# Optimization experiments

Hardware: AMD Instinct MI355X
Metric: run time of the kernel (lower is better)

## Reference

```python
import jax, jax.numpy as jnp
import numpy as np


def setup_inputs() -> dict:
    key = jax.random.key(0)
    kp, ka = jax.random.split(key)
    N, A = 100000, 1024
    # points: xyz over a 100m x 100m plot, z in [0, 30] (tree heights)
    u = jax.random.uniform(kp, (N, 3), dtype=jnp.float32)
    points = u * jnp.array([100.0, 100.0, 30.0], dtype=jnp.float32)
    # anchors: [cx, cy, cz, w, l, h]
    ua = jax.random.uniform(ka, (A, 6), dtype=jnp.float32)
    cx = ua[:, 0] * 100.0
    cy = ua[:, 1] * 100.0
    cz = jnp.zeros((A,), jnp.float32)
    w = 2.0 + ua[:, 3] * 6.0
    l = 2.0 + ua[:, 4] * 6.0
    h = 10.0 + ua[:, 5] * 20.0
    anchors = jnp.stack([cx, cy, cz, w, l, h], axis=1)
    return {"points": points, "anchors": anchors, "n": 512}


def _roi_point_pool(points, anchors, n):
    """Vectorised per-anchor point-in-box pooling (TreeRCNN._subsample_points_batch).

    Returns padded [A, n, 3] anchor-local points (x,y translated by anchor
    center, z untouched) and per-anchor clamped counts. Slots >= count are 0.
    Selection of the first-n in-box points is deterministic in point order
    (the torch code uses a random tie-break key; determinism chosen for a
    reproducible correctness baseline — same gather/scatter structure).
    """
    A = anchors.shape[0]
    N = points.shape[0]
    px, py, pz = points[:, 0], points[:, 1], points[:, 2]
    cx, cy = anchors[:, 0:1], anchors[:, 1:2]
    w, l, h = anchors[:, 3:4], anchors[:, 4:5], anchors[:, 5:6]
    # [A, N] box-membership mask (the O(A*N) traffic-bound hot loop)
    mask = ((px >= cx - w * 0.5) & (px <= cx + w * 0.5)
            & (py >= cy - l * 0.5) & (py <= cy + l * 0.5)
            & (pz >= 0.0) & (pz <= h))
    # per-anchor local slot index for each in-box point
    local = jnp.cumsum(mask.astype(jnp.int32), axis=1) - 1          # [A, N]
    valid = mask & (local < n)
    counts = valid.sum(axis=1)                                      # [A]
    # scatter point ids (+1 so 0 marks empty) into flat padded slots;
    # invalid hits go to a dump slot A*n
    flat = jnp.where(valid,
                     jnp.arange(A, dtype=jnp.int32)[:, None] * n + local,
                     A * n)
    vals = (jnp.arange(N, dtype=jnp.int32)[None, :] + 1) * valid
    pid = jnp.zeros(A * n + 1, jnp.int32).at[flat.reshape(-1)].add(vals.reshape(-1))
    pid = pid[: A * n].reshape(A, n)                                # [A, n]
    points_ext = jnp.concatenate([jnp.zeros((1, 3), points.dtype), points], axis=0)
    padded = points_ext[pid]                                        # [A, n, 3]
    # translate x,y to anchor-local coords on filled slots only
    centers = jnp.concatenate([anchors[:, :2], jnp.zeros((A, 1), anchors.dtype)], axis=1)
    padded = jnp.where(pid[..., None] > 0, padded - centers[:, None, :], 0.0)
    return padded, counts


def reference(points, anchors, n):
    return _roi_point_pool(points, anchors, n)
```

## Files before the change

### kernel.cpp

```cpp
#include <hip/hip_runtime.h>


#define NB     128
#define NBB    (NB * NB)
#define CAPB   32
#define NWRD   3584
#define WPT    7
#define MAXBIN 160

__global__ __launch_bounds__(256) void scatter_kernel(
    const float* __restrict__ pts, unsigned int* __restrict__ bincnt,
    float4* __restrict__ bucket, const unsigned int* __restrict__ pbase, int N)
{
    const int i = blockIdx.x * 256 + threadIdx.x;
    if (i >= N) return;
    const unsigned int P = *pbase;
    const float px = pts[3 * i + 0], py = pts[3 * i + 1], pz = pts[3 * i + 2];
    const float s = NB / 100.0f;
    const int bx = min(NB - 1, (int)(px * s));
    const int by = min(NB - 1, (int)(py * s));
    const int bin = by * NB + bx;
    const unsigned int slot = atomicAdd(&bincnt[bin], 1u) - P;
    if (slot < CAPB)
        bucket[bin * CAPB + slot] = make_float4(px, py, pz, __int_as_float(i));
}

__global__ __launch_bounds__(512) void anchor_kernel(
    const float* __restrict__ pts, const float* __restrict__ anc,
    const unsigned int* __restrict__ bincnt, const float4* __restrict__ bucket,
    const unsigned int* __restrict__ pbase,
    float* __restrict__ out_pts, float* __restrict__ out_cnt, int n)
{
    const int a    = blockIdx.x;
    const int tid  = threadIdx.x;
    const int lane = tid & 63;
    const int wave = tid >> 6;

    const float cx = anc[a * 6 + 0], cy = anc[a * 6 + 1];
    const float w  = anc[a * 6 + 3], l  = anc[a * 6 + 4], h = anc[a * 6 + 5];
    const float xl = cx - w * 0.5f, xh = cx + w * 0.5f;
    const float yl = cy - l * 0.5f, yh = cy + l * 0.5f;

    __shared__ unsigned int s_mask[NWRD];
    __shared__ int s_bcnt[MAXBIN];
    __shared__ int s_wsum[8], s_wpre[9];

    #pragma unroll
    for (int u = 0; u < WPT; ++u) s_mask[tid + u * 512] = 0u;

    const unsigned int P = *pbase;
    const float sc = NB / 100.0f;
    const int bx0 = max(0, (int)floorf(xl * sc));
    const int bx1 = min(NB - 1, (int)floorf(xh * sc));
    const int by0 = max(0, (int)floorf(yl * sc));
    const int by1 = min(NB - 1, (int)floorf(yh * sc));
    const int nbx = bx1 - bx0 + 1;
    const int nby = by1 - by0 + 1;
    const int nbins = (nbx > 0 && nby > 0) ? nbx * nby : 0;

    for (int t = tid; t < nbins; t += 512) {
        const int by = by0 + t / nbx, bx = bx0 + t % nbx;
        s_bcnt[t] = min((int)(bincnt[by * NB + bx] - P), CAPB);
    }
    __syncthreads();

    const int totB = nbins * 8;
    for (int t = tid; t < totB; t += 512) {
        const int slot = t & 7;
        const int b    = t >> 3;
        const int cnt  = s_bcnt[b];
        const int bin  = (by0 + b / nbx) * NB + bx0 + b % nbx;
        const float4 p = bucket[bin * CAPB + slot];
        if (slot < cnt &&
            p.x >= xl && p.x <= xh && p.y >= yl && p.y <= yh &&
            p.z >= 0.0f && p.z <= h) {
            const int idx = __float_as_int(p.w);
            atomicOr(&s_mask[idx >> 5], 1u << (idx & 31));
        }
    }

    const int totC = nbins * 24;
    for (int t = tid; t < totC; t += 512) {
        const int b    = t / 24;
        const int slot = 8 + t - b * 24;
        const int cnt  = s_bcnt[b];
        if (slot < cnt) {
            const int bin  = (by0 + b / nbx) * NB + bx0 + b % nbx;
            const float4 p = bucket[bin * CAPB + slot];
            if (p.x >= xl && p.x <= xh && p.y >= yl && p.y <= yh &&
                p.z >= 0.0f && p.z <= h) {
                const int idx = __float_as_int(p.w);
                atomicOr(&s_mask[idx >> 5], 1u << (idx & 31));
            }
        }
    }
    __syncthreads();

    const int wbase = tid * WPT;
    int s = 0;
    unsigned int mw[WPT];
    #pragma unroll
    for (int u = 0; u < WPT; ++u) {
        mw[u] = s_mask[wbase + u];
        s += __popc(mw[u]);
    }
    int incl = s;
    #pragma unroll
    for (int d = 1; d < 64; d <<= 1) {
        const int t = __shfl_up(incl, d);
        if (lane >= d) incl += t;
    }
    if (lane == 63) s_wsum[wave] = incl;
    __syncthreads();
    if (tid == 0) {
        int run = 0;
        #pragma unroll
        for (int v = 0; v < 8; ++v) { const int t = s_wsum[v]; s_wpre[v] = run; run += t; }
        s_wpre[8] = run;
    }
    __syncthreads();
    const int total = s_wpre[8];
    const int count = total < n ? total : n;
    int slot = s_wpre[wave] + incl - s;

    float* const outa = out_pts + (size_t)a * n * 3;
    #pragma unroll
    for (int u = 0; u < WPT; ++u) {
        unsigned int wm = mw[u];
        while (wm) {
            const int b = __ffs(wm) - 1;
            wm &= wm - 1u;
            if (slot < n) {
                const int i = (wbase + u) * 32 + b;
                outa[3 * slot + 0] = pts[3 * i + 0] - cx;
                outa[3 * slot + 1] = pts[3 * i + 1] - cy;
                outa[3 * slot + 2] = pts[3 * i + 2];
            }
            ++slot;
        }
    }

    for (int t = count * 3 + tid; t < n * 3; t += 512) outa[t] = 0.f;
    if (tid == 0) out_cnt[a] = (float)count;
}

__global__ __launch_bounds__(256) void roi_pool_kernel(
    const float* __restrict__ pts, const float* __restrict__ anc,
    float* __restrict__ out_pts, float* __restrict__ out_cnt, int N, int n)
{
    const int a = blockIdx.x;
    const float cx = anc[a * 6 + 0], cy = anc[a * 6 + 1];
    const float w  = anc[a * 6 + 3], l  = anc[a * 6 + 4], h = anc[a * 6 + 5];
    const float xmin = cx - 0.5f * w, xmax = cx + 0.5f * w;
    const float ymin = cy - 0.5f * l, ymax = cy + 0.5f * l;
    const int tid = threadIdx.x, wave = tid >> 6, lane = tid & 63;
    __shared__ int s_tot[4];
    int base = 0;
    float* const outa = out_pts + (size_t)a * n * 3;
    for (int start = 0; start < N; start += 256) {
        const int i = start + tid;
        bool m = false;
        float px = 0.f, py = 0.f, pz = 0.f;
        if (i < N) {
            px = pts[3 * i]; py = pts[3 * i + 1]; pz = pts[3 * i + 2];
            m = (px >= xmin) & (px <= xmax) & (py >= ymin) & (py <= ymax) &
                (pz >= 0.0f) & (pz <= h);
        }
        const unsigned long long ball = __ballot(m);
        const int lanePfx = __popcll(ball & ((1ull << lane) - 1ull));
        if (lane == 0) s_tot[wave] = __popcll(ball);
        __syncthreads();
        const int t0 = s_tot[0], t1 = s_tot[1], t2 = s_tot[2], t3 = s_tot[3];
        int offs = base;
        if (wave > 0) offs += t0;
        if (wave > 1) offs += t1;
        if (wave > 2) offs += t2;
        const int slot = offs + lanePfx;
        if (m && slot < n) {
            float* o = outa + (size_t)slot * 3;
            o[0] = px - cx; o[1] = py - cy; o[2] = pz;
        }
        base += t0 + t1 + t2 + t3;
        __syncthreads();
        if (base >= n) break;
    }
    const int count = base < n ? base : n;
    if (tid == 0) out_cnt[a] = (float)count;
    for (int s = count + tid; s < n; s += 256) {
        float* o = outa + (size_t)s * 3;
        o[0] = 0.f; o[1] = 0.f; o[2] = 0.f;
    }
}

extern "C" void kernel_launch(void* const* d_in, const int* in_sizes, int n_in,
                              void* d_out, int out_size, void* d_ws, size_t ws_size,
                              hipStream_t stream) {
    const float* pts = (const float*)d_in[0];
    const float* anc = (const float*)d_in[1];
    const int N = in_sizes[0] / 3;
    const int A = in_sizes[1] / 6;
    const int n = (out_size / A - 1) / 3;

    float* out_pts = (float*)d_out;
    float* out_cnt = (float*)d_out + (size_t)A * n * 3;

    const size_t bucket_bytes = (size_t)NBB * CAPB * sizeof(float4);
    const size_t cnt_bytes    = (size_t)NBB * sizeof(int);
    const size_t total_ws     = bucket_bytes + cnt_bytes + 64;

    if (ws_size < total_ws || N > NWRD * 32) {
        roi_pool_kernel<<<dim3(A), dim3(256), 0, stream>>>(pts, anc, out_pts, out_cnt, N, n);
        return;
    }

    float4* bucket       = (float4*)d_ws;
    unsigned int* bincnt = (unsigned int*)((char*)d_ws + bucket_bytes);
    const unsigned int* pbase =
        (const unsigned int*)((char*)d_ws + bucket_bytes + cnt_bytes);

    const int pb = (N + 255) / 256;

    scatter_kernel<<<dim3(pb), dim3(256), 0, stream>>>(pts, bincnt, bucket, pbase, N);
    anchor_kernel<<<dim3(A), dim3(512), 0, stream>>>(pts, anc, bincnt, bucket, pbase,
                                                     out_pts, out_cnt, n);
}
```

Measured before the change: 77.65 us.

## Process anchor pairs per block and emit hits directly via rank lookup

The anchor kernel now handles two anchors per block. It prefetches the first 16 slots of each bin into registers, and issues the second anchor's bucket loads while the first anchor is still emitting, so memory latency overlaps with work. Output is no longer produced by walking the mask bits and re-gathering points from the original array. Each hit computes its rank from a per-word prefix array plus a popcount and writes its output directly. The cost is roughly four times the LDS per block (about 57 KB), which lowers occupancy, half as many blocks for the 1024 anchors, and serial handling of the two anchors within a block.

```diff
diff --git a/kernel.cpp b/kernel.cpp
--- a/kernel.cpp
+++ b/kernel.cpp
@@ -25,123 +25,231 @@
         bucket[bin * CAPB + slot] = make_float4(px, py, pz, __int_as_float(i));
 }
 
-__global__ __launch_bounds__(512) void anchor_kernel(
-    const float* __restrict__ pts, const float* __restrict__ anc,
+struct Win {
+    float xl, xh, yl, yh, h, cx, cy;
+    int bx0, by0, nbx, nbins;
+};
+
+__device__ __forceinline__ Win make_win(const float* __restrict__ anc, int a) {
+    Win W;
+    W.cx = anc[a * 6 + 0]; W.cy = anc[a * 6 + 1];
+    const float w = anc[a * 6 + 3], l = anc[a * 6 + 4];
+    W.h = anc[a * 6 + 5];
+    W.xl = W.cx - w * 0.5f; W.xh = W.cx + w * 0.5f;
+    W.yl = W.cy - l * 0.5f; W.yh = W.cy + l * 0.5f;
+    const float sc = NB / 100.0f;
+    const int bx0 = max(0, (int)floorf(W.xl * sc));
+    const int bx1 = min(NB - 1, (int)floorf(W.xh * sc));
+    const int by0 = max(0, (int)floorf(W.yl * sc));
+    const int by1 = min(NB - 1, (int)floorf(W.yh * sc));
+    W.bx0 = bx0; W.by0 = by0;
+    W.nbx = bx1 - bx0 + 1;
+    const int nby = by1 - by0 + 1;
+    W.nbins = (W.nbx > 0 && nby > 0) ? W.nbx * nby : 0;
+    return W;
+}
+
+__device__ __forceinline__ void stage_bcnt(const Win& W,
+    const unsigned int* __restrict__ bincnt, unsigned int P, int* s_b, int tid)
+{
+    for (int t = tid; t < W.nbins; t += 512) {
+        const int by = W.by0 + t / W.nbx, bx = W.bx0 + t % W.nbx;
+        s_b[t] = min((int)(bincnt[by * NB + bx] - P), CAPB);
+    }
+}
+
+__device__ __forceinline__ void issue_payload(const Win& W,
+    const float4* __restrict__ bucket, int tid, float4* pB, float4* pC)
+{
+    const int totB = W.nbins * 8;
+    #pragma unroll
+    for (int k = 0; k < 3; ++k) {
+        const int t = tid + k * 512;
+        if (t < totB) {
+            const int b = t >> 3;
+            const int off =
+                ((W.by0 + b / W.nbx) * NB + W.bx0 + b % W.nbx) * CAPB + (t & 7);
+            pB[k] = bucket[off];
+            pC[k] = bucket[off + 8];
+        }
+    }
+}
+
+__device__ __forceinline__ bool testp(const Win& W, const float4 p) {
+    return p.x >= W.xl && p.x <= W.xh && p.y >= W.yl && p.y <= W.yh &&
+           p.z >= 0.0f && p.z <= W.h;
+}
+
+__device__ __forceinline__ void set_bits(const Win& W, const int* s_b,
+    const float4* pB, const float4* pC, unsigned int* s_m, int tid)
+{
+    const int totB = W.nbins * 8;
+    #pragma unroll
+    for (int k = 0; k < 3; ++k) {
+        const int t = tid + k * 512;
+        if (t < totB) {
+            const int cnt = s_b[t >> 3];
+            const int sl  = t & 7;
+            if (sl < cnt && testp(W, pB[k])) {
+                const int idx = __float_as_int(pB[k].w);
+                atomicOr(&s_m[idx >> 5], 1u << (idx & 31));
+            }
+            if (sl + 8 < cnt && testp(W, pC[k])) {
+                const int idx = __float_as_int(pC[k].w);
+                atomicOr(&s_m[idx >> 5], 1u << (idx & 31));
+            }
+        }
+    }
+}
+
+__device__ __forceinline__ void phasec_set(const Win& W, const int* s_b,
+    const float4* __restrict__ bucket, unsigned int* s_m, int tid)
+{
+    const int totC = W.nbins * 16;
+    for (int t = tid; t < totC; t += 512) {
+        const int b = t >> 4, slot = 16 + (t & 15);
+        if (slot < s_b[b]) {
+            const int bin = (W.by0 + b / W.nbx) * NB + W.bx0 + b % W.nbx;
+            const float4 p = bucket[bin * CAPB + slot];
+            if (testp(W, p)) {
+                const int idx = __float_as_int(p.w);
+                atomicOr(&s_m[idx >> 5], 1u << (idx & 31));
+            }
+        }
+    }
+}
+
+__device__ __forceinline__ int scan_rank(const unsigned int* s_m,
+    unsigned int* s_wp, int* s_ws, int tid, int lane, int wave)
+{
+    const int wbase = tid * WPT;
+    unsigned int mw[WPT];
+    int s = 0;
+    #pragma unroll
+    for (int u = 0; u < WPT; ++u) {
+        mw[u] = s_m[wbase + u];
+        s += __popc(mw[u]);
+    }
+    int incl = s;
+    #pragma unroll
+    for (int d = 1; d < 64; d <<= 1) {
+        const int t = __shfl_up(incl, d);
+        if (lane >= d) incl += t;
+    }
+    if (lane == 63) s_ws[wave] = incl;
+    __syncthreads();
+    int pre = 0, total = 0;
+    #pragma unroll
+    for (int v = 0; v < 8; ++v) {
+        const int t = s_ws[v];
+        if (v < wave) pre += t;
+        total += t;
+    }
+    unsigned int run = (unsigned int)(pre + incl - s);
+    #pragma unroll
+    for (int u = 0; u < WPT; ++u) {
+        s_wp[wbase + u] = run;
+        run += (unsigned int)__popc(mw[u]);
+    }
+    __syncthreads();
+    return total;
+}
+
+__device__ __forceinline__ void emit_one(const Win& W, const float4 p,
+    const unsigned int* s_m, const unsigned int* s_wp, int n, float* outa)
+{
+    const int idx = __float_as_int(p.w);
+    const int wd  = idx >> 5;
+    const int rank = (int)s_wp[wd] + __popc(s_m[wd] & ((1u << (idx & 31)) - 1u));
+    if (rank < n) {
+        outa[3 * rank + 0] = p.x - W.cx;
+        outa[3 * rank + 1] = p.y - W.cy;
+        outa[3 * rank + 2] = p.z;
+    }
+}
+
+__device__ __forceinline__ void emit_hits(const Win& W, const int* s_b,
+    const float4* pB, const float4* pC, const float4* __restrict__ bucket,
+    const unsigned int* s_m, const unsigned int* s_wp, int tid, int n,
+    float* outa)
+{
+    const int totB = W.nbins * 8;
+    #pragma unroll
+    for (int k = 0; k < 3; ++k) {
+        const int t = tid + k * 512;
+        if (t < totB) {
+            const int cnt = s_b[t >> 3];
+            const int sl  = t & 7;
+            if (sl < cnt && testp(W, pB[k])) emit_one(W, pB[k], s_m, s_wp, n, outa);
+            if (sl + 8 < cnt && testp(W, pC[k])) emit_one(W, pC[k], s_m, s_wp, n, outa);
+        }
+    }
+    const int totC = W.nbins * 16;
+    for (int t = tid; t < totC; t += 512) {
+        const int b = t >> 4, slot = 16 + (t & 15);
+        if (slot < s_b[b]) {
+            const int bin = (W.by0 + b / W.nbx) * NB + W.bx0 + b % W.nbx;
+            const float4 p = bucket[bin * CAPB + slot];
+            if (testp(W, p)) emit_one(W, p, s_m, s_wp, n, outa);
+        }
+    }
+}
+
+__global__ __launch_bounds__(512, 4) void anchor_pair_kernel(
+    const float* __restrict__ anc,
     const unsigned int* __restrict__ bincnt, const float4* __restrict__ bucket,
     const unsigned int* __restrict__ pbase,
-    float* __restrict__ out_pts, float* __restrict__ out_cnt, int n)
-{
-    const int a    = blockIdx.x;
+    float* __restrict__ out_pts, float* __restrict__ out_cnt, int n, int A)
+{
+    const int a0   = blockIdx.x * 2, a1 = a0 + 1;
     const int tid  = threadIdx.x;
     const int lane = tid & 63;
     const int wave = tid >> 6;
 
-    const float cx = anc[a * 6 + 0], cy = anc[a * 6 + 1];
-    const float w  = anc[a * 6 + 3], l  = anc[a * 6 + 4], h = anc[a * 6 + 5];
-    const float xl = cx - w * 0.5f, xh = cx + w * 0.5f;
-    const float yl = cy - l * 0.5f, yh = cy + l * 0.5f;
-
-    __shared__ unsigned int s_mask[NWRD];
-    __shared__ int s_bcnt[MAXBIN];
-    __shared__ int s_wsum[8], s_wpre[9];
-
-    #pragma unroll
-    for (int u = 0; u < WPT; ++u) s_mask[tid + u * 512] = 0u;
+    __shared__ unsigned int s_maskA[NWRD], s_wpreA[NWRD];
+    __shared__ unsigned int s_maskB[NWRD], s_wpreB[NWRD];
+    __shared__ int s_b0[MAXBIN], s_b1[MAXBIN], s_ws[8];
+
+    const bool two = (a1 < A);
+
+    #pragma unroll
+    for (int u = 0; u < WPT; ++u) {
+        s_maskA[tid + u * 512] = 0u;
+        s_maskB[tid + u * 512] = 0u;
+    }
 
     const unsigned int P = *pbase;
-    const float sc = NB / 100.0f;
-    const int bx0 = max(0, (int)floorf(xl * sc));
-    const int bx1 = min(NB - 1, (int)floorf(xh * sc));
-    const int by0 = max(0, (int)floorf(yl * sc));
-    const int by1 = min(NB - 1, (int)floorf(yh * sc));
-    const int nbx = bx1 - bx0 + 1;
-    const int nby = by1 - by0 + 1;
-    const int nbins = (nbx > 0 && nby > 0) ? nbx * nby : 0;
-
-    for (int t = tid; t < nbins; t += 512) {
-        const int by = by0 + t / nbx, bx = bx0 + t % nbx;
-        s_bcnt[t] = min((int)(bincnt[by * NB + bx] - P), CAPB);
-    }
-    __syncthreads();
-
-    const int totB = nbins * 8;
-    for (int t = tid; t < totB; t += 512) {
-        const int slot = t & 7;
-        const int b    = t >> 3;
-        const int cnt  = s_bcnt[b];
-        const int bin  = (by0 + b / nbx) * NB + bx0 + b % nbx;
-        const float4 p = bucket[bin * CAPB + slot];
-        if (slot < cnt &&
-            p.x >= xl && p.x <= xh && p.y >= yl && p.y <= yh &&
-            p.z >= 0.0f && p.z <= h) {
-            const int idx = __float_as_int(p.w);
-            atomicOr(&s_mask[idx >> 5], 1u << (idx & 31));
-        }
-    }
-
-    const int totC = nbins * 24;
-    for (int t = tid; t < totC; t += 512) {
-        const int b    = t / 24;
-        const int slot = 8 + t - b * 24;
-        const int cnt  = s_bcnt[b];
-        if (slot < cnt) {
-            const int bin  = (by0 + b / nbx) * NB + bx0 + b % nbx;
-            const float4 p = bucket[bin * CAPB + slot];
-            if (p.x >= xl && p.x <= xh && p.y >= yl && p.y <= yh &&
-                p.z >= 0.0f && p.z <= h) {
-                const int idx = __float_as_int(p.w);
-                atomicOr(&s_mask[idx >> 5], 1u << (idx & 31));
-            }
-        }
-    }
-    __syncthreads();
-
-    const int wbase = tid * WPT;
-    int s = 0;
-    unsigned int mw[WPT];
-    #pragma unroll
-    for (int u = 0; u < WPT; ++u) {
-        mw[u] = s_mask[wbase + u];
-        s += __popc(mw[u]);
-    }
-    int incl = s;
-    #pragma unroll
-    for (int d = 1; d < 64; d <<= 1) {
-        const int t = __shfl_up(incl, d);
-        if (lane >= d) incl += t;
-    }
-    if (lane == 63) s_wsum[wave] = incl;
-    __syncthreads();
-    if (tid == 0) {
-        int run = 0;
-        #pragma unroll
-        for (int v = 0; v < 8; ++v) { const int t = s_wsum[v]; s_wpre[v] = run; run += t; }
-        s_wpre[8] = run;
-    }
-    __syncthreads();
-    const int total = s_wpre[8];
-    const int count = total < n ? total : n;
-    int slot = s_wpre[wave] + incl - s;
-
-    float* const outa = out_pts + (size_t)a * n * 3;
-    #pragma unroll
-    for (int u = 0; u < WPT; ++u) {
-        unsigned int wm = mw[u];
-        while (wm) {
-            const int b = __ffs(wm) - 1;
-            wm &= wm - 1u;
-            if (slot < n) {
-                const int i = (wbase + u) * 32 + b;
-                outa[3 * slot + 0] = pts[3 * i + 0] - cx;
-                outa[3 * slot + 1] = pts[3 * i + 1] - cy;
-                outa[3 * slot + 2] = pts[3 * i + 2];
-            }
-            ++slot;
-        }
-    }
-
-    for (int t = count * 3 + tid; t < n * 3; t += 512) outa[t] = 0.f;
-    if (tid == 0) out_cnt[a] = (float)count;
+
+    const Win W0 = make_win(anc, a0);
+    stage_bcnt(W0, bincnt, P, s_b0, tid);
+    Win W1;
+    if (two) { W1 = make_win(anc, a1); stage_bcnt(W1, bincnt, P, s_b1, tid); }
+    float4 pB[3], pC[3];
+    issue_payload(W0, bucket, tid, pB, pC);
+    __syncthreads();
+
+    set_bits(W0, s_b0, pB, pC, s_maskA, tid);
+    phasec_set(W0, s_b0, bucket, s_maskA, tid);
+    __syncthreads();
+    const int total0 = scan_rank(s_maskA, s_wpreA, s_ws, tid, lane, wave);
+    const int count0 = total0 < n ? total0 : n;
+    float* const outa0 = out_pts + (size_t)a0 * n * 3;
+    emit_hits(W0, s_b0, pB, pC, bucket, s_maskA, s_wpreA, tid, n, outa0);
+    if (two) issue_payload(W1, bucket, tid, pB, pC);
+    for (int t = count0 * 3 + tid; t < n * 3; t += 512) outa0[t] = 0.f;
+    if (tid == 0) out_cnt[a0] = (float)count0;
+
+    if (!two) return;
+
+    set_bits(W1, s_b1, pB, pC, s_maskB, tid);
+    phasec_set(W1, s_b1, bucket, s_maskB, tid);
+    __syncthreads();
+    const int total1 = scan_rank(s_maskB, s_wpreB, s_ws, tid, lane, wave);
+    const int count1 = total1 < n ? total1 : n;
+    float* const outa1 = out_pts + (size_t)a1 * n * 3;
+    emit_hits(W1, s_b1, pB, pC, bucket, s_maskB, s_wpreB, tid, n, outa1);
+    for (int t = count1 * 3 + tid; t < n * 3; t += 512) outa1[t] = 0.f;
+    if (tid == 0) out_cnt[a1] = (float)count1;
 }
 
 __global__ __launch_bounds__(256) void roi_pool_kernel(
@@ -219,8 +327,9 @@
         (const unsigned int*)((char*)d_ws + bucket_bytes + cnt_bytes);
 
     const int pb = (N + 255) / 256;
+    const int ab = (A + 1) / 2;
 
     scatter_kernel<<<dim3(pb), dim3(256), 0, stream>>>(pts, bincnt, bucket, pbase, N);
-    anchor_kernel<<<dim3(A), dim3(512), 0, stream>>>(pts, anc, bincnt, bucket, pbase,
-                                                     out_pts, out_cnt, n);
-}
+    anchor_pair_kernel<<<dim3(ab), dim3(512), 0, stream>>>(anc, bincnt, bucket, pbase,
+                                                           out_pts, out_cnt, n, A);
+}
```

New measurement: 74.09 us. -4.6%, faster.
